# Optimization experiments

Measured on AMD Instinct MI355X. Metric: run time of the kernel, lower is better.

## Reference

```python
import jax, jax.numpy as jnp
import numpy as np

FP16_HUGE = 2.0 ** 15
NUM_HEAD = 4
LN_EPS = 1e-5


def setup_inputs() -> dict:
    key = jax.random.key(0)
    ks = jax.random.split(key, 12)
    B, N, D = 1, 256, 128
    H = NUM_HEAD
    inp = {
        "pair_act": jax.random.normal(ks[0], (B, N, N, D), dtype=jnp.float32),
        "pair_mask": jnp.ones((B, N, N), dtype=jnp.float32),
        "ln_scale": jnp.ones((D,), dtype=jnp.float32),
        "ln_bias": jnp.zeros((D,), dtype=jnp.float32),
        # torch Linear weight layout: [out_dim, in_dim]; applied as x @ W.T
        "w2d": jax.random.normal(ks[1], (H, D), dtype=jnp.float32) / np.sqrt(D),
        "wq": jax.random.normal(ks[2], (D, D), dtype=jnp.float32) / np.sqrt(D),
        "wk": jax.random.normal(ks[3], (D, D), dtype=jnp.float32) / np.sqrt(D),
        "wv": jax.random.normal(ks[4], (D, D), dtype=jnp.float32) / np.sqrt(D),
        "wg": jax.random.normal(ks[5], (D, D), dtype=jnp.float32) / np.sqrt(D),
        "bg": jnp.ones((D,), dtype=jnp.float32),  # gating bias init = 1.0
        "wo": jax.random.normal(ks[6], (D, D), dtype=jnp.float32) * 0.02,
        "bo": jnp.zeros((D,), dtype=jnp.float32),
    }
    return inp


def reference(pair_act, pair_mask, ln_scale, ln_bias, w2d, wq, wk, wv, wg, bg, wo, bo):
    B, N, _, D = pair_act.shape
    H = NUM_HEAD
    kd = D // H  # per-head key/value dim
    scale = kd ** (-0.5)

    # mask bias: [B, N(row), 1, 1, N(key)]
    bias = (FP16_HUGE * (pair_mask - 1.0))[:, :, None, None, :]

    # LayerNorm (fp32, eps=1e-5)
    mu = jnp.mean(pair_act, axis=-1, keepdims=True)
    var = jnp.mean(jnp.square(pair_act - mu), axis=-1, keepdims=True)
    x = (pair_act - mu) * jax.lax.rsqrt(var + LN_EPS) * ln_scale + ln_bias

    # non-batched per-head bias: [B, 1, H, N, N]
    nb = jnp.einsum("bijd,hd->bhij", x, w2d)[:, None]

    q = (x @ wq.T).reshape(B, N, N, H, kd) * scale  # [B, r, i, H, kd]
    k = (x @ wk.T).reshape(B, N, N, H, kd)
    v = (x @ wv.T).reshape(B, N, N, H, kd)

    logits = jnp.einsum("brihk,brjhk->brhij", q, k) + bias + nb  # [B, r, H, i, j]
    w = jax.nn.softmax(logits, axis=-1)
    o = jnp.einsum("brhij,brjhv->brihv", w, v)  # [B, r, i, H, kd]

    g = jax.nn.sigmoid(x @ wg.T + bg).reshape(B, N, N, H, kd)
    o = (o * g).reshape(B, N, N, D)

    out = o @ wo.T + bo
    return out * pair_mask[..., None]
```

## Files before the change

### kernel.cpp

```cpp
#include <hip/hip_runtime.h>
#include <hip/hip_bf16.h>

typedef unsigned short u16;
typedef __attribute__((ext_vector_type(8))) short bf16x8;
typedef __attribute__((ext_vector_type(4))) float f32x4;
typedef __attribute__((address_space(3))) unsigned lds_u32;
typedef const __attribute__((address_space(1))) unsigned glb_u32;

#define N 256
#define D 128
#define NH 4
#define KD 32
#define NN 65536
#define QK_SCALE 0.17677669529663687f
#define HUGE_MASK 32768.0f

__device__ __forceinline__ float b2f(u16 s) {
  union { float f; unsigned u; } x; x.u = ((unsigned)s) << 16; return x.f;
}
__device__ __forceinline__ u16 f2b(float f) {
  union { float f; unsigned u; } x; x.f = f;
  unsigned r = x.u + 0x7fff + ((x.u >> 16) & 1);
  return (u16)(r >> 16);
}

__global__ __launch_bounds__(256) void prep_w_kernel(
    const float* __restrict__ wq, const float* __restrict__ wk,
    const float* __restrict__ wv, const float* __restrict__ wg,
    const float* __restrict__ wo, u16* __restrict__ wb)
{
  int idx = blockIdx.x * 256 + threadIdx.x;
  const float* srcs[5] = {wq, wk, wv, wg, wo};
  int mat = idx >> 11, rem = idx & 2047;
  int row = rem >> 4, g = rem & 15;
  int gp = (g + (row & 15)) & 15;
  const float* s = srcs[mat] + row * 128 + g * 8;
  float4 f0 = *(const float4*)(s);
  float4 f1 = *(const float4*)(s + 4);
  uint4 pk;
  pk.x = (unsigned)f2b(f0.x) | ((unsigned)f2b(f0.y) << 16);
  pk.y = (unsigned)f2b(f0.z) | ((unsigned)f2b(f0.w) << 16);
  pk.z = (unsigned)f2b(f1.x) | ((unsigned)f2b(f1.y) << 16);
  pk.w = (unsigned)f2b(f1.z) | ((unsigned)f2b(f1.w) << 16);
  *(uint4*)(wb + (size_t)mat * 16384 + row * 128 + gp * 8) = pk;
}

__device__ __forceinline__ void async_stage(const u16* __restrict__ gsrc, u16* lds, int tid) {
  int lane = tid & 63, wave = tid >> 6;
  u16* lbase = lds + wave * 512;
  const u16* gbase = gsrc + wave * 512 + lane * 8;
#pragma unroll
  for (int p = 0; p < 8; p++) {
    __builtin_amdgcn_global_load_lds((glb_u32*)(gbase + p * 2048),
                                     (lds_u32*)(lbase + p * 2048), 16, 0, 0);
  }
}

__global__ __launch_bounds__(256) void projln_kernel(
    const float* __restrict__ pa, const float* __restrict__ lns, const float* __restrict__ lnb,
    const float* __restrict__ w2d, const u16* __restrict__ wb, const float* __restrict__ bg,
    u16* __restrict__ q, u16* __restrict__ k, u16* __restrict__ v, u16* __restrict__ g,
    float* __restrict__ nbT)
{
  __shared__ __align__(16) u16 Wl[2][16384];
  int tid = threadIdx.x;
  int wave = tid >> 6, lane = tid & 63;
  int lr = lane & 15, quad = lane >> 4;

  async_stage(wb, Wl[0], tid);

  bf16x8 a[2][4];
#pragma unroll
  for (int mt = 0; mt < 2; mt++) {
    int row = blockIdx.x * 128 + wave * 32 + mt * 16 + lr;
    const float* rp = pa + (size_t)row * D;
    float xv[4][8];
    float s = 0.f, ss = 0.f;
#pragma unroll
    for (int ks = 0; ks < 4; ks++) {
      float4 a0 = *(const float4*)(rp + ks * 32 + quad * 8);
      float4 a1 = *(const float4*)(rp + ks * 32 + quad * 8 + 4);
      xv[ks][0] = a0.x; xv[ks][1] = a0.y; xv[ks][2] = a0.z; xv[ks][3] = a0.w;
      xv[ks][4] = a1.x; xv[ks][5] = a1.y; xv[ks][6] = a1.z; xv[ks][7] = a1.w;
#pragma unroll
      for (int j = 0; j < 8; j++) { s += xv[ks][j]; ss += xv[ks][j] * xv[ks][j]; }
    }
    s  += __shfl_xor(s, 16, 64);  ss += __shfl_xor(ss, 16, 64);
    s  += __shfl_xor(s, 32, 64);  ss += __shfl_xor(ss, 32, 64);
    float mu = s * (1.0f / D);
    float var = ss * (1.0f / D) - mu * mu;
    float rs = rsqrtf(var + 1e-5f);
#pragma unroll
    for (int ks = 0; ks < 4; ks++) {
      float4 s0 = *(const float4*)(lns + ks * 32 + quad * 8);
      float4 s1 = *(const float4*)(lns + ks * 32 + quad * 8 + 4);
      float4 b0 = *(const float4*)(lnb + ks * 32 + quad * 8);
      float4 b1 = *(const float4*)(lnb + ks * 32 + quad * 8 + 4);
      float sc[8] = {s0.x,s0.y,s0.z,s0.w,s1.x,s1.y,s1.z,s1.w};
      float bi[8] = {b0.x,b0.y,b0.z,b0.w,b1.x,b1.y,b1.z,b1.w};
#pragma unroll
      for (int j = 0; j < 8; j++) xv[ks][j] = (xv[ks][j] - mu) * rs * sc[j] + bi[j];
    }
#pragma unroll
    for (int h = 0; h < NH; h++) {
      float p = 0.f;
#pragma unroll
      for (int ks = 0; ks < 4; ks++) {
        float4 w0 = *(const float4*)(w2d + h * D + ks * 32 + quad * 8);
        float4 w1 = *(const float4*)(w2d + h * D + ks * 32 + quad * 8 + 4);
        p += xv[ks][0]*w0.x + xv[ks][1]*w0.y + xv[ks][2]*w0.z + xv[ks][3]*w0.w
           + xv[ks][4]*w1.x + xv[ks][5]*w1.y + xv[ks][6]*w1.z + xv[ks][7]*w1.w;
      }
      p += __shfl_xor(p, 16, 64);
      p += __shfl_xor(p, 32, 64);
      if (quad == 0)
        nbT[(size_t)h * NN + (size_t)(row & 255) * 256 + (row >> 8)] = p;
    }
#pragma unroll
    for (int ks = 0; ks < 4; ks++)
#pragma unroll
      for (int j = 0; j < 8; j++) a[mt][ks][j] = (short)f2b(xv[ks][j]);
  }
  __syncthreads();

  u16* Os[4] = {q, k, v, g};
#pragma unroll
  for (int mat = 0; mat < 4; mat++) {
    if (mat < 3) async_stage(wb + (size_t)(mat + 1) * 16384, Wl[(mat + 1) & 1], tid);
    const u16* Wcur = Wl[mat & 1];
    f32x4 acc[2][2][4];
#pragma unroll
    for (int mt = 0; mt < 2; mt++)
#pragma unroll
      for (int tg = 0; tg < 2; tg++)
#pragma unroll
        for (int e = 0; e < 4; e++) acc[mt][tg][e] = (f32x4){0.f, 0.f, 0.f, 0.f};
#pragma unroll
    for (int ks = 0; ks < 4; ks++) {
#pragma unroll
      for (int tg = 0; tg < 2; tg++) {
#pragma unroll
        for (int e = 0; e < 4; e++) {
          int nrow = tg * 64 + 4 * lr + e;
          int gp = (ks * 4 + quad + (nrow & 15)) & 15;
          bf16x8 b = *(const bf16x8*)(&Wcur[nrow * 128 + gp * 8]);
          acc[0][tg][e] = __builtin_amdgcn_mfma_f32_16x16x32_bf16(a[0][ks], b, acc[0][tg][e], 0, 0, 0);
          acc[1][tg][e] = __builtin_amdgcn_mfma_f32_16x16x32_bf16(a[1][ks], b, acc[1][tg][e], 0, 0, 0);
        }
      }
    }
    u16* O = Os[mat];
#pragma unroll
    for (int mt = 0; mt < 2; mt++) {
      int row0 = blockIdx.x * 128 + wave * 32 + mt * 16 + quad * 4;
#pragma unroll
      for (int tg = 0; tg < 2; tg++) {
        int c0 = tg * 64 + 4 * lr;
        float bg0 = 0.f, bg1 = 0.f, bg2 = 0.f, bg3 = 0.f;
        if (mat == 3) { bg0 = bg[c0]; bg1 = bg[c0+1]; bg2 = bg[c0+2]; bg3 = bg[c0+3]; }
#pragma unroll
        for (int reg = 0; reg < 4; reg++) {
          float v0 = acc[mt][tg][0][reg], v1 = acc[mt][tg][1][reg];
          float v2 = acc[mt][tg][2][reg], v3 = acc[mt][tg][3][reg];
          if (mat == 0) { v0 *= QK_SCALE; v1 *= QK_SCALE; v2 *= QK_SCALE; v3 *= QK_SCALE; }
          if (mat == 3) {
            v0 = 1.0f / (1.0f + __expf(-(v0 + bg0)));
            v1 = 1.0f / (1.0f + __expf(-(v1 + bg1)));
            v2 = 1.0f / (1.0f + __expf(-(v2 + bg2)));
            v3 = 1.0f / (1.0f + __expf(-(v3 + bg3)));
          }
          uint2 pk;
          pk.x = (unsigned)f2b(v0) | ((unsigned)f2b(v1) << 16);
          pk.y = (unsigned)f2b(v2) | ((unsigned)f2b(v3) << 16);
          *(uint2*)(O + (size_t)(row0 + reg) * D + c0) = pk;
        }
      }
    }
    __syncthreads();
  }
}

__global__ __launch_bounds__(256) void attn_kernel(
    const u16* __restrict__ q, const u16* __restrict__ k, const u16* __restrict__ v,
    const u16* __restrict__ g, const float* __restrict__ nbT, const float* __restrict__ mask,
    u16* __restrict__ og)
{
  __shared__ __align__(16) u16 Kf[8192];
  __shared__ __align__(16) u16 Vf[8192];
  __shared__ __align__(16) u16 Pf[16384];
  __shared__ float bias_lds[256];
  int h = blockIdx.x & 3, r = blockIdx.x >> 2;
  int tid = threadIdx.x;
  {
    int j = tid;
    const u16* krow = k + ((size_t)r * N + j) * D + h * KD;
    int t = j >> 4, lrj = j & 15;
#pragma unroll
    for (int qc = 0; qc < 4; qc++)
      *(bf16x8*)(&Kf[((t * 4 + qc) * 16 + lrj) * 8]) = *(const bf16x8*)(krow + qc * 8);
    const u16* vrow = v + ((size_t)r * N + j) * D + h * KD;
    int ks = j >> 5, qj = (j >> 3) & 3, jj = j & 7;
#pragma unroll
    for (int c = 0; c < 32; c++)
      Vf[(((ks * 2 + (c & 1)) * 4 + qj) * 16 + (c >> 1)) * 8 + jj] = vrow[c];
    bias_lds[tid] = HUGE_MASK * (mask[r * N + tid] - 1.0f);
  }
  __syncthreads();
  int wave = tid >> 6, lane = tid & 63;
  int lr = lane & 15, quad = lane >> 4;
  u16* Pw = &Pf[wave * 4096];
  float bias_v[16];
#pragma unroll
  for (int t = 0; t < 16; t++) bias_v[t] = bias_lds[t * 16 + lr];
  const float* nbh = nbT + (size_t)h * NN;

  for (int pass = 0; pass < 4; pass++) {
    int i0 = pass * 64 + wave * 16;
    bf16x8 af = *(const bf16x8*)(q + ((size_t)r * N + i0 + lr) * D + h * KD + quad * 8);
    f32x4 S[16];
#pragma unroll
    for (int t = 0; t < 16; t++) {
      bf16x8 bfr = *(const bf16x8*)(&Kf[((t * 4 + quad) * 16 + lr) * 8]);
      S[t] = __builtin_amdgcn_mfma_f32_16x16x32_bf16(af, bfr, (f32x4){0.f,0.f,0.f,0.f}, 0, 0, 0);
    }
    float mx[4] = {-3e38f, -3e38f, -3e38f, -3e38f};
#pragma unroll
    for (int t = 0; t < 16; t++) {
      float4 nb4 = *(const float4*)(nbh + (size_t)(t * 16 + lr) * N + i0 + quad * 4);
      float bl = bias_v[t];
      S[t][0] += nb4.x + bl;  S[t][1] += nb4.y + bl;
      S[t][2] += nb4.z + bl;  S[t][3] += nb4.w + bl;
      mx[0] = fmaxf(mx[0], S[t][0]); mx[1] = fmaxf(mx[1], S[t][1]);
      mx[2] = fmaxf(mx[2], S[t][2]); mx[3] = fmaxf(mx[3], S[t][3]);
    }
#pragma unroll
    for (int reg = 0; reg < 4; reg++) {
#pragma unroll
      for (int off = 8; off; off >>= 1)
        mx[reg] = fmaxf(mx[reg], __shfl_xor(mx[reg], off, 16));
    }
    float lsum[4] = {0.f, 0.f, 0.f, 0.f};
#pragma unroll
    for (int t = 0; t < 16; t++) {
      int j = t * 16 + lr;
      int cbase = ((j >> 5) * 4 + ((j >> 3) & 3)) * 128 + (j & 7);
#pragma unroll
      for (int reg = 0; reg < 4; reg++) {
        float p = __expf(S[t][reg] - mx[reg]);
        lsum[reg] += p;
        union { float f; unsigned u; } cv; cv.f = p;
        Pw[cbase + (quad * 4 + reg) * 8] = (u16)((cv.u + 0x8000u) >> 16);
      }
    }
#pragma unroll
    for (int reg = 0; reg < 4; reg++) {
#pragma unroll
      for (int off = 8; off; off >>= 1)
        lsum[reg] += __shfl_xor(lsum[reg], off, 16);
    }
    __asm__ __volatile__("s_waitcnt lgkmcnt(0)" ::: "memory");
    f32x4 o[2] = {(f32x4){0.f,0.f,0.f,0.f}, (f32x4){0.f,0.f,0.f,0.f}};
#pragma unroll
    for (int ks = 0; ks < 8; ks++) {
      bf16x8 pa = *(const bf16x8*)(&Pw[((ks * 4 + quad) * 16 + lr) * 8]);
#pragma unroll
      for (int e = 0; e < 2; e++) {
        bf16x8 vb = *(const bf16x8*)(&Vf[(((ks * 2 + e) * 4 + quad) * 16 + lr) * 8]);
        o[e] = __builtin_amdgcn_mfma_f32_16x16x32_bf16(pa, vb, o[e], 0, 0, 0);
      }
    }
#pragma unroll
    for (int reg = 0; reg < 4; reg++) {
      float inv = __builtin_amdgcn_rcpf(lsum[reg]);
      int i = i0 + quad * 4 + reg;
      size_t base = ((size_t)r * N + i) * D + h * KD + 2 * lr;
      unsigned gv = *(const unsigned*)(g + base);
      float r0 = o[0][reg] * inv * b2f((u16)(gv & 0xffff));
      float r1 = o[1][reg] * inv * b2f((u16)(gv >> 16));
      *(unsigned*)(og + base) = (unsigned)f2b(r0) | ((unsigned)f2b(r1) << 16);
    }
  }
}

__global__ __launch_bounds__(256) void out_kernel(
    const u16* __restrict__ og, const u16* __restrict__ wob, const float* __restrict__ bo,
    const float* __restrict__ mask, float* __restrict__ out)
{
  __shared__ __align__(16) u16 Wlds[16384];
  int tid = threadIdx.x;
  async_stage(wob, Wlds, tid);
  int wave = tid >> 6, lane = tid & 63;
  int lr = lane & 15, quad = lane >> 4;
  bf16x8 a[2][4];
#pragma unroll
  for (int mt = 0; mt < 2; mt++) {
    int arow = blockIdx.x * 128 + wave * 32 + mt * 16 + lr;
#pragma unroll
    for (int ks = 0; ks < 4; ks++)
      a[mt][ks] = *(const bf16x8*)(og + (size_t)arow * D + ks * 32 + quad * 8);
  }
  __syncthreads();
  f32x4 acc[2][2][4];
#pragma unroll
  for (int mt = 0; mt < 2; mt++)
#pragma unroll
    for (int tg = 0; tg < 2; tg++)
#pragma unroll
      for (int e = 0; e < 4; e++) acc[mt][tg][e] = (f32x4){0.f, 0.f, 0.f, 0.f};
#pragma unroll
  for (int ks = 0; ks < 4; ks++) {
#pragma unroll
    for (int tg = 0; tg < 2; tg++) {
#pragma unroll
      for (int e = 0; e < 4; e++) {
        int nrow = tg * 64 + 4 * lr + e;
        int gp = (ks * 4 + quad + (nrow & 15)) & 15;
        bf16x8 b = *(const bf16x8*)(&Wlds[nrow * 128 + gp * 8]);
        acc[0][tg][e] = __builtin_amdgcn_mfma_f32_16x16x32_bf16(a[0][ks], b, acc[0][tg][e], 0, 0, 0);
        acc[1][tg][e] = __builtin_amdgcn_mfma_f32_16x16x32_bf16(a[1][ks], b, acc[1][tg][e], 0, 0, 0);
      }
    }
  }
#pragma unroll
  for (int mt = 0; mt < 2; mt++) {
    int row0 = blockIdx.x * 128 + wave * 32 + mt * 16 + quad * 4;
#pragma unroll
    for (int tg = 0; tg < 2; tg++) {
      int c0 = tg * 64 + 4 * lr;
      float4 bo4 = *(const float4*)(bo + c0);
#pragma unroll
      for (int reg = 0; reg < 4; reg++) {
        int pos = row0 + reg;
        float m = mask[pos];
        float4 o4;
        o4.x = (acc[mt][tg][0][reg] + bo4.x) * m;
        o4.y = (acc[mt][tg][1][reg] + bo4.y) * m;
        o4.z = (acc[mt][tg][2][reg] + bo4.z) * m;
        o4.w = (acc[mt][tg][3][reg] + bo4.w) * m;
        *(float4*)(out + (size_t)pos * D + c0) = o4;
      }
    }
  }
}

extern "C" void kernel_launch(void* const* d_in, const int* in_sizes, int n_in,
                              void* d_out, int out_size, void* d_ws, size_t ws_size,
                              hipStream_t stream)
{
  const float* pa   = (const float*)d_in[0];
  const float* mask = (const float*)d_in[1];
  const float* lns  = (const float*)d_in[2];
  const float* lnb  = (const float*)d_in[3];
  const float* w2d  = (const float*)d_in[4];
  const float* wq   = (const float*)d_in[5];
  const float* wk   = (const float*)d_in[6];
  const float* wv   = (const float*)d_in[7];
  const float* wg   = (const float*)d_in[8];
  const float* bg   = (const float*)d_in[9];
  const float* wo   = (const float*)d_in[10];
  const float* bo   = (const float*)d_in[11];

  const size_t ARR = (size_t)NN * D;
  u16* q  = (u16*)d_ws;
  u16* k  = q + ARR;
  u16* v  = k + ARR;
  u16* g  = v + ARR;
  u16* og = g + ARR;
  float* nbT = (float*)(og + ARR);
  u16* wb = (u16*)(nbT + (size_t)NH * NN);

  prep_w_kernel<<<40, 256, 0, stream>>>(wq, wk, wv, wg, wo, wb);
  projln_kernel<<<512, 256, 0, stream>>>(pa, lns, lnb, w2d, wb, bg, q, k, v, g, nbT);
  attn_kernel<<<N * NH, 256, 0, stream>>>(q, k, v, g, nbT, mask, og);
  out_kernel<<<512, 256, 0, stream>>>(og, wb + 4 * 16384, bo, mask, (float*)d_out);
}
```

Baseline: 187.6 us.

## Transpose attention MFMA operands so softmax reduces in-lane, halve P buffer

Swaps the MFMA operand order for the QK^T and PV products so each lane holds a full query row's logits. The row max and sum then reduce mostly inside the lane, with two cross-lane shuffles instead of per-register 16-lane shuffle trees. The pair bias is stored untransposed so the attention kernel reads it contiguously per row. P is written in two halves with packed 8-byte LDS stores, halving the P buffer, and the V staging loop is rotated per lane group to reduce LDS bank conflicts. Output gating is done with one 16-byte load and store per lane; the added complexity raises correctness risk in the operand layouts.

```diff
diff --git a/kernel.cpp b/kernel.cpp
--- a/kernel.cpp
+++ b/kernel.cpp
@@ -60,7 +60,7 @@
     const float* __restrict__ pa, const float* __restrict__ lns, const float* __restrict__ lnb,
     const float* __restrict__ w2d, const u16* __restrict__ wb, const float* __restrict__ bg,
     u16* __restrict__ q, u16* __restrict__ k, u16* __restrict__ v, u16* __restrict__ g,
-    float* __restrict__ nbT)
+    float* __restrict__ nb)
 {
   __shared__ __align__(16) u16 Wl[2][16384];
   int tid = threadIdx.x;
@@ -113,8 +113,7 @@
       }
       p += __shfl_xor(p, 16, 64);
       p += __shfl_xor(p, 32, 64);
-      if (quad == 0)
-        nbT[(size_t)h * NN + (size_t)(row & 255) * 256 + (row >> 8)] = p;
+      if (quad == 0) nb[(size_t)h * NN + row] = p;
     }
 #pragma unroll
     for (int ks = 0; ks < 4; ks++)
@@ -182,12 +181,12 @@
 
 __global__ __launch_bounds__(256) void attn_kernel(
     const u16* __restrict__ q, const u16* __restrict__ k, const u16* __restrict__ v,
-    const u16* __restrict__ g, const float* __restrict__ nbT, const float* __restrict__ mask,
+    const u16* __restrict__ g, const float* __restrict__ nb, const float* __restrict__ mask,
     u16* __restrict__ og)
 {
   __shared__ __align__(16) u16 Kf[8192];
   __shared__ __align__(16) u16 Vf[8192];
-  __shared__ __align__(16) u16 Pf[16384];
+  __shared__ __align__(16) u16 Pf[8192];
   __shared__ float bias_lds[256];
   int h = blockIdx.x & 3, r = blockIdx.x >> 2;
   int tid = threadIdx.x;
@@ -201,18 +200,16 @@
     const u16* vrow = v + ((size_t)r * N + j) * D + h * KD;
     int ks = j >> 5, qj = (j >> 3) & 3, jj = j & 7;
 #pragma unroll
-    for (int c = 0; c < 32; c++)
+    for (int cc = 0; cc < 32; cc++) {
+      int c = (cc + qj * 8) & 31;
       Vf[(((ks * 2 + (c & 1)) * 4 + qj) * 16 + (c >> 1)) * 8 + jj] = vrow[c];
+    }
     bias_lds[tid] = HUGE_MASK * (mask[r * N + tid] - 1.0f);
   }
   __syncthreads();
   int wave = tid >> 6, lane = tid & 63;
   int lr = lane & 15, quad = lane >> 4;
-  u16* Pw = &Pf[wave * 4096];
-  float bias_v[16];
-#pragma unroll
-  for (int t = 0; t < 16; t++) bias_v[t] = bias_lds[t * 16 + lr];
-  const float* nbh = nbT + (size_t)h * NN;
+  u16* Pw = &Pf[wave * 2048];
 
   for (int pass = 0; pass < 4; pass++) {
     int i0 = pass * 64 + wave * 16;
@@ -220,65 +217,68 @@
     f32x4 S[16];
 #pragma unroll
     for (int t = 0; t < 16; t++) {
-      bf16x8 bfr = *(const bf16x8*)(&Kf[((t * 4 + quad) * 16 + lr) * 8]);
-      S[t] = __builtin_amdgcn_mfma_f32_16x16x32_bf16(af, bfr, (f32x4){0.f,0.f,0.f,0.f}, 0, 0, 0);
-    }
-    float mx[4] = {-3e38f, -3e38f, -3e38f, -3e38f};
+      bf16x8 kf = *(const bf16x8*)(&Kf[((t * 4 + quad) * 16 + lr) * 8]);
+      S[t] = __builtin_amdgcn_mfma_f32_16x16x32_bf16(kf, af, (f32x4){0.f,0.f,0.f,0.f}, 0, 0, 0);
+    }
+    const float* nbrow = nb + (size_t)h * NN + (size_t)(i0 + lr) * N;
+    float mx = -3e38f;
 #pragma unroll
     for (int t = 0; t < 16; t++) {
-      float4 nb4 = *(const float4*)(nbh + (size_t)(t * 16 + lr) * N + i0 + quad * 4);
-      float bl = bias_v[t];
-      S[t][0] += nb4.x + bl;  S[t][1] += nb4.y + bl;
-      S[t][2] += nb4.z + bl;  S[t][3] += nb4.w + bl;
-      mx[0] = fmaxf(mx[0], S[t][0]); mx[1] = fmaxf(mx[1], S[t][1]);
-      mx[2] = fmaxf(mx[2], S[t][2]); mx[3] = fmaxf(mx[3], S[t][3]);
-    }
+      float4 nb4 = *(const float4*)(nbrow + t * 16 + quad * 4);
+      float4 b4 = *(const float4*)(&bias_lds[t * 16 + quad * 4]);
+      S[t][0] += nb4.x + b4.x;  S[t][1] += nb4.y + b4.y;
+      S[t][2] += nb4.z + b4.z;  S[t][3] += nb4.w + b4.w;
+      mx = fmaxf(mx, fmaxf(fmaxf(S[t][0], S[t][1]), fmaxf(S[t][2], S[t][3])));
+    }
+    mx = fmaxf(mx, __shfl_xor(mx, 16, 64));
+    mx = fmaxf(mx, __shfl_xor(mx, 32, 64));
+    float lsum = 0.f;
+    f32x4 o[2] = {(f32x4){0.f,0.f,0.f,0.f}, (f32x4){0.f,0.f,0.f,0.f}};
+#pragma unroll
+    for (int hf = 0; hf < 2; hf++) {
+      __asm__ __volatile__("s_waitcnt lgkmcnt(0)" ::: "memory");
+#pragma unroll
+      for (int tt = 0; tt < 8; tt++) {
+        int t = hf * 8 + tt;
+        float e0 = __expf(S[t][0] - mx), e1 = __expf(S[t][1] - mx);
+        float e2 = __expf(S[t][2] - mx), e3 = __expf(S[t][3] - mx);
+        lsum += (e0 + e1) + (e2 + e3);
+        union { float f; unsigned u; } c0, c1, c2, c3;
+        c0.f = e0; c1.f = e1; c2.f = e2; c3.f = e3;
+        uint2 pk;
+        pk.x = ((c0.u + 0x8000u) >> 16) | ((c1.u + 0x8000u) & 0xffff0000u);
+        pk.y = ((c2.u + 0x8000u) >> 16) | ((c3.u + 0x8000u) & 0xffff0000u);
+        int ksl = tt >> 1;
+        int qc = (2 * t + (quad >> 1)) & 3;
+        *(uint2*)(&Pw[((ksl * 4 + qc) * 16 + lr) * 8 + 4 * (quad & 1)]) = pk;
+      }
+      __asm__ __volatile__("s_waitcnt lgkmcnt(0)" ::: "memory");
+#pragma unroll
+      for (int ks = 0; ks < 4; ks++) {
+        int ksg = hf * 4 + ks;
+        bf16x8 pb = *(const bf16x8*)(&Pw[((ks * 4 + quad) * 16 + lr) * 8]);
+#pragma unroll
+        for (int e = 0; e < 2; e++) {
+          bf16x8 vb = *(const bf16x8*)(&Vf[(((ksg * 2 + e) * 4 + quad) * 16 + lr) * 8]);
+          o[e] = __builtin_amdgcn_mfma_f32_16x16x32_bf16(vb, pb, o[e], 0, 0, 0);
+        }
+      }
+    }
+    lsum += __shfl_xor(lsum, 16, 64);
+    lsum += __shfl_xor(lsum, 32, 64);
+    float inv = __builtin_amdgcn_rcpf(lsum);
+    size_t base = ((size_t)r * N + i0 + lr) * D + h * KD + quad * 8;
+    bf16x8 gv = *(const bf16x8*)(g + base);
+    bf16x8 pk8;
 #pragma unroll
     for (int reg = 0; reg < 4; reg++) {
 #pragma unroll
-      for (int off = 8; off; off >>= 1)
-        mx[reg] = fmaxf(mx[reg], __shfl_xor(mx[reg], off, 16));
-    }
-    float lsum[4] = {0.f, 0.f, 0.f, 0.f};
-#pragma unroll
-    for (int t = 0; t < 16; t++) {
-      int j = t * 16 + lr;
-      int cbase = ((j >> 5) * 4 + ((j >> 3) & 3)) * 128 + (j & 7);
-#pragma unroll
-      for (int reg = 0; reg < 4; reg++) {
-        float p = __expf(S[t][reg] - mx[reg]);
-        lsum[reg] += p;
-        union { float f; unsigned u; } cv; cv.f = p;
-        Pw[cbase + (quad * 4 + reg) * 8] = (u16)((cv.u + 0x8000u) >> 16);
-      }
-    }
-#pragma unroll
-    for (int reg = 0; reg < 4; reg++) {
-#pragma unroll
-      for (int off = 8; off; off >>= 1)
-        lsum[reg] += __shfl_xor(lsum[reg], off, 16);
-    }
-    __asm__ __volatile__("s_waitcnt lgkmcnt(0)" ::: "memory");
-    f32x4 o[2] = {(f32x4){0.f,0.f,0.f,0.f}, (f32x4){0.f,0.f,0.f,0.f}};
-#pragma unroll
-    for (int ks = 0; ks < 8; ks++) {
-      bf16x8 pa = *(const bf16x8*)(&Pw[((ks * 4 + quad) * 16 + lr) * 8]);
-#pragma unroll
       for (int e = 0; e < 2; e++) {
-        bf16x8 vb = *(const bf16x8*)(&Vf[(((ks * 2 + e) * 4 + quad) * 16 + lr) * 8]);
-        o[e] = __builtin_amdgcn_mfma_f32_16x16x32_bf16(pa, vb, o[e], 0, 0, 0);
-      }
-    }
-#pragma unroll
-    for (int reg = 0; reg < 4; reg++) {
-      float inv = __builtin_amdgcn_rcpf(lsum[reg]);
-      int i = i0 + quad * 4 + reg;
-      size_t base = ((size_t)r * N + i) * D + h * KD + 2 * lr;
-      unsigned gv = *(const unsigned*)(g + base);
-      float r0 = o[0][reg] * inv * b2f((u16)(gv & 0xffff));
-      float r1 = o[1][reg] * inv * b2f((u16)(gv >> 16));
-      *(unsigned*)(og + base) = (unsigned)f2b(r0) | ((unsigned)f2b(r1) << 16);
-    }
+        float val = o[e][reg] * inv * b2f((u16)gv[2 * reg + e]);
+        pk8[2 * reg + e] = (short)f2b(val);
+      }
+    }
+    *(bf16x8*)(og + base) = pk8;
   }
 }
 
@@ -366,11 +366,11 @@
   u16* v  = k + ARR;
   u16* g  = v + ARR;
   u16* og = g + ARR;
-  float* nbT = (float*)(og + ARR);
-  u16* wb = (u16*)(nbT + (size_t)NH * NN);
+  float* nb = (float*)(og + ARR);
+  u16* wb = (u16*)(nb + (size_t)NH * NN);
 
   prep_w_kernel<<<40, 256, 0, stream>>>(wq, wk, wv, wg, wo, wb);
-  projln_kernel<<<512, 256, 0, stream>>>(pa, lns, lnb, w2d, wb, bg, q, k, v, g, nbT);
-  attn_kernel<<<N * NH, 256, 0, stream>>>(q, k, v, g, nbT, mask, og);
+  projln_kernel<<<512, 256, 0, stream>>>(pa, lns, lnb, w2d, wb, bg, q, k, v, g, nb);
+  attn_kernel<<<N * NH, 256, 0, stream>>>(q, k, v, g, nb, mask, og);
   out_kernel<<<512, 256, 0, stream>>>(og, wb + 4 * 16384, bo, mask, (float*)d_out);
 }
```

Result: slower. 208.5 us (+11.1%).
